# Optimization experiments

Measured on AMD Instinct MI355X. Metric: run time of the kernel, lower is better.

Reference implementation:

```python
import jax, jax.numpy as jnp
import numpy as np

D_MODEL = 1024
D_STATE = 128
SEQ_LEN = 4096
BATCH = 4
N_FFT = 2 ** int(np.ceil(np.log2(2 * SEQ_LEN - 1)))  # 8192
LN_EPS = 1e-3  # keras LayerNormalization default epsilon


def setup_inputs() -> dict:
    key = jax.random.key(0)
    ks = jax.random.split(key, 12)
    def dense_w(k, fan_in, fan_out):
        lim = np.sqrt(6.0 / (fan_in + fan_out)).astype(np.float32)  # glorot uniform
        return jax.random.uniform(k, (fan_in, fan_out), jnp.float32, -lim, lim)
    return {
        "x": jax.random.normal(ks[0], (BATCH, SEQ_LEN, D_MODEL), jnp.float32),
        "ln_gamma": jnp.ones((D_MODEL,), jnp.float32),
        "ln_beta": jnp.zeros((D_MODEL,), jnp.float32),
        "W_in": dense_w(ks[1], D_MODEL, D_MODEL),
        "b_in": jnp.zeros((D_MODEL,), jnp.float32),
        "W_xs": dense_w(ks[2], D_MODEL, D_STATE),
        "W_B": dense_w(ks[3], D_MODEL, D_STATE),
        "b_B": jnp.zeros((D_STATE,), jnp.float32),
        "W_C": dense_w(ks[4], D_MODEL, D_STATE),
        "b_C": jnp.zeros((D_STATE,), jnp.float32),
        "A_log": jax.random.uniform(ks[5], (D_STATE,), jnp.float32, -4.0, -1.0),
        "D": jnp.ones((D_MODEL,), jnp.float32),
        "W_so": dense_w(ks[6], D_STATE, D_MODEL),
        "W_out": dense_w(ks[7], D_MODEL, D_MODEL),
        "b_out": jnp.zeros((D_MODEL,), jnp.float32),
    }


def reference(x, ln_gamma, ln_beta, W_in, b_in, W_xs, W_B, b_B, W_C, b_C,
              A_log, D, W_so, W_out, b_out):
    residual = x
    # LayerNorm over last dim
    mu = jnp.mean(x, axis=-1, keepdims=True)
    var = jnp.mean(jnp.square(x - mu), axis=-1, keepdims=True)
    xn = (x - mu) * jax.lax.rsqrt(var + LN_EPS) * ln_gamma + ln_beta
    # projections
    z = xn @ W_in + b_in                      # [B, L, d_model]
    x_state = z @ W_xs                        # [B, L, d_state]
    B_sel = z @ W_B + b_B                     # [B, L, d_state]
    C_sel = z @ W_C + b_C                     # [B, L, d_state]
    # stable A-parameterization -> kernel K[t, s] = exp(A_s * t)
    A = -jnp.exp(A_log)                       # [d_state]
    t = jnp.arange(SEQ_LEN, dtype=jnp.float32)
    K = jnp.exp(t[:, None] * A[None, :])      # [L, d_state]
    # FFT convolution along time axis (zero-padded to N_FFT, causal slice)
    u = x_state * B_sel                       # [B, L, d_state]
    u_f = jnp.fft.rfft(u, n=N_FFT, axis=1)    # [B, N_FFT//2+1, d_state]
    k_f = jnp.fft.rfft(K, n=N_FFT, axis=0)    # [N_FFT//2+1, d_state]
    y_state = jnp.fft.irfft(u_f * k_f[None], n=N_FFT, axis=1)[:, :SEQ_LEN]
    y_state = y_state * C_sel
    # output path with skip connection through D
    y = y_state @ W_so + D * z                # [B, L, d_model]
    y = y @ W_out + b_out
    return y + residual
```

## Files before the change

### kernel.cpp

```cpp
#include <hip/hip_runtime.h>
#include <math.h>

#define D_MODEL 1024
#define D_STATE 128
#define SEQ_LEN 4096
#define BATCH 4
#define NTOK (BATCH * SEQ_LEN)
#define LN_EPS 1e-3f
#define NCHUNK 128
#define LCHUNK (SEQ_LEN / NCHUNK)

typedef __attribute__((ext_vector_type(8))) short bf16x8;
typedef __attribute__((ext_vector_type(4))) float f32x4;

__device__ __forceinline__ short f2bf(float f) {
    union { float f; unsigned u; } v; v.f = f;
    unsigned r = v.u + 0x7FFFu + ((v.u >> 16) & 1u);
    return (short)(r >> 16);
}
__device__ __forceinline__ float bf2f(short s) {
    union { unsigned u; float f; } v; v.u = ((unsigned)(unsigned short)s) << 16;
    return v.f;
}

__global__ __launch_bounds__(256) void ln_kernel(const float* __restrict__ x,
                                                 const float* __restrict__ gamma,
                                                 const float* __restrict__ beta,
                                                 short* __restrict__ xn_bf) {
    int row = blockIdx.x;
    const float4* xr = (const float4*)(x + (size_t)row * D_MODEL);
    float4 v = xr[threadIdx.x];
    float s1 = v.x + v.y + v.z + v.w;
    float s2 = v.x * v.x + v.y * v.y + v.z * v.z + v.w * v.w;
    for (int off = 32; off; off >>= 1) {
        s1 += __shfl_down(s1, off);
        s2 += __shfl_down(s2, off);
    }
    __shared__ float ls1[4], ls2[4];
    int wid = threadIdx.x >> 6, lane = threadIdx.x & 63;
    if (lane == 0) { ls1[wid] = s1; ls2[wid] = s2; }
    __syncthreads();
    s1 = ls1[0] + ls1[1] + ls1[2] + ls1[3];
    s2 = ls2[0] + ls2[1] + ls2[2] + ls2[3];
    float mu = s1 * (1.0f / D_MODEL);
    float var = s2 * (1.0f / D_MODEL) - mu * mu;
    float r = rsqrtf(var + LN_EPS);
    float4 g = ((const float4*)gamma)[threadIdx.x];
    float4 b = ((const float4*)beta)[threadIdx.x];
    short4 o;
    o.x = f2bf((v.x - mu) * r * g.x + b.x);
    o.y = f2bf((v.y - mu) * r * g.y + b.y);
    o.z = f2bf((v.z - mu) * r * g.z + b.z);
    o.w = f2bf((v.w - mu) * r * g.w + b.w);
    ((short4*)(xn_bf + (size_t)row * D_MODEL))[threadIdx.x] = o;
}

__global__ __launch_bounds__(256) void prep_kernel(
    const float* __restrict__ W_in, const float* __restrict__ W_xs,
    const float* __restrict__ W_B, const float* __restrict__ W_C,
    const float* __restrict__ W_so, const float* __restrict__ W_out,
    const float* __restrict__ bB, const float* __restrict__ bC,
    short* __restrict__ W_inT, short* __restrict__ W3T,
    short* __restrict__ W_soT, short* __restrict__ W_outT,
    float* __restrict__ bias3) {
    int blk = blockIdx.x;
    const float* in; short* out; int K, N, tile;
    if (blk < 1024)      { in = W_in;  out = W_inT;           K = 1024; N = 1024; tile = blk; }
    else if (blk < 1152) { in = W_xs;  out = W3T;             K = 1024; N = 128;  tile = blk - 1024; }
    else if (blk < 1280) { in = W_B;   out = W3T + 128*1024;  K = 1024; N = 128;  tile = blk - 1152; }
    else if (blk < 1408) { in = W_C;   out = W3T + 256*1024;  K = 1024; N = 128;  tile = blk - 1280; }
    else if (blk < 1536) { in = W_so;  out = W_soT;           K = 128;  N = 1024; tile = blk - 1408; }
    else if (blk < 2560) { in = W_out; out = W_outT;          K = 1024; N = 1024; tile = blk - 1536; }
    else {
        int t = threadIdx.y * 32 + threadIdx.x;
        for (int n = t; n < 384; n += 256)
            bias3[n] = (n < 128) ? 0.f : ((n < 256) ? bB[n - 128] : bC[n - 256]);
        return;
    }
    __shared__ float t32[32][33];
    int ntiles = N / 32;
    int nb = (tile % ntiles) * 32, kb = (tile / ntiles) * 32;
    int tx = threadIdx.x, ty = threadIdx.y;
#pragma unroll
    for (int i = 0; i < 4; ++i)
        t32[ty + 8 * i][tx] = in[(size_t)(kb + ty + 8 * i) * N + nb + tx];
    __syncthreads();
#pragma unroll
    for (int i = 0; i < 4; ++i)
        out[(size_t)(nb + ty + 8 * i) * K + kb + tx] = f2bf(t32[tx][ty + 8 * i]);
}

template<int HAS_BIAS, int HAS_ADD, int ADD_BF, int HAS_SCALE, int OUT_F32, int OUT_BF, int SWZ>
__global__ __launch_bounds__(256, 4) void gemm_bf16(
    const short* __restrict__ A, const short* __restrict__ BT,
    const float* __restrict__ bias,
    const float* __restrict__ addf, const short* __restrict__ addb,
    const float* __restrict__ addscale,
    float* __restrict__ Cf, short* __restrict__ Cbf,
    int Mt, int Nt, int K) {
    __shared__ short As[128 * 64];
    __shared__ short Bs[128 * 64];
    int p = blockIdx.x;
    int mtile, ntile;
    if (SWZ) {
        int k = p & 7, q = p >> 3;
        ntile = q & 7;
        mtile = k + 8 * (q >> 3);
    } else {
        mtile = p % Mt;
        ntile = p / Mt;
    }
    int m0 = mtile * 128, n0 = ntile * 128;
    int N = Nt * 128;
    int tid = threadIdx.x;
    int lane = tid & 63;
    int w = tid >> 6;
    int quad = lane >> 4, r16 = lane & 15;
    int wm = (w & 1) * 64, wn = (w >> 1) * 64;

    f32x4 acc[4][4] = {};

    for (int k0 = 0; k0 < K; k0 += 64) {
#pragma unroll
        for (int it = 0; it < 4; ++it) {
            int seg = it * 256 + tid;
            int row = seg >> 3, slot = seg & 7;
            int kc8 = slot ^ (row & 7);
            const short* gp = A + (size_t)(m0 + row) * K + k0 + kc8 * 8;
            __builtin_amdgcn_global_load_lds(
                (const __attribute__((address_space(1))) unsigned*)gp,
                (__attribute__((address_space(3))) unsigned*)(As + seg * 8), 16, 0, 0);
        }
#pragma unroll
        for (int it = 0; it < 4; ++it) {
            int seg = it * 256 + tid;
            int row = seg >> 3, slot = seg & 7;
            int kc8 = slot ^ (row & 7);
            const short* gp = BT + (size_t)(n0 + row) * K + k0 + kc8 * 8;
            __builtin_amdgcn_global_load_lds(
                (const __attribute__((address_space(1))) unsigned*)gp,
                (__attribute__((address_space(3))) unsigned*)(Bs + seg * 8), 16, 0, 0);
        }
        __syncthreads();

        const short* abase = As + (wm + r16) * 64;
        const short* bbase = Bs + (wn + r16) * 64;
        int sw = r16 & 7;
#pragma unroll
        for (int kk = 0; kk < 2; ++kk) {
            int phys = ((quad + 4 * kk) ^ sw) * 8;
            bf16x8 af[4], bfr[4];
#pragma unroll
            for (int i = 0; i < 4; ++i) af[i] = *(const bf16x8*)(abase + i * 16 * 64 + phys);
#pragma unroll
            for (int j = 0; j < 4; ++j) bfr[j] = *(const bf16x8*)(bbase + j * 16 * 64 + phys);
#pragma unroll
            for (int i = 0; i < 4; ++i)
#pragma unroll
                for (int j = 0; j < 4; ++j)
                    acc[i][j] = __builtin_amdgcn_mfma_f32_16x16x32_bf16(af[i], bfr[j], acc[i][j], 0, 0, 0);
        }
        __syncthreads();
    }

#pragma unroll
    for (int i = 0; i < 4; ++i) {
#pragma unroll
        for (int j = 0; j < 4; ++j) {
            int col = n0 + wn + j * 16 + r16;
            float bv = HAS_BIAS ? bias[col] : 0.f;
            float sc = HAS_SCALE ? addscale[col] : 1.f;
#pragma unroll
            for (int pr = 0; pr < 4; ++pr) {
                int row = m0 + wm + i * 16 + quad * 4 + pr;
                float v = acc[i][j][pr] + bv;
                if (HAS_ADD) {
                    float av = ADD_BF ? bf2f(addb[(size_t)row * N + col])
                                      : addf[(size_t)row * N + col];
                    v += sc * av;
                }
                if (OUT_F32) Cf[(size_t)row * N + col] = v;
                if (OUT_BF) Cbf[(size_t)row * N + col] = f2bf(v);
            }
        }
    }
}

__global__ __launch_bounds__(128) void scan_p1(const float* __restrict__ s3,
                                               const float* __restrict__ A_log,
                                               float* __restrict__ hbuf,
                                               float* __restrict__ Ebuf) {
    int s = threadIdx.x;
    int c = blockIdx.x, b = blockIdx.y;
    float a = expf(-expf(A_log[s]));
    float h = 0.f;
    size_t base = (size_t)b * SEQ_LEN + (size_t)c * LCHUNK;
#pragma unroll 8
    for (int i = 0; i < LCHUNK; ++i) {
        size_t r = base + i;
        float u = s3[r * 384 + s] * s3[r * 384 + 128 + s];
        h = a * h + u;
        hbuf[r * 128 + s] = h;
    }
    Ebuf[((size_t)b * NCHUNK + c) * 128 + s] = h;
}

__global__ __launch_bounds__(512) void scan_p2(const float* __restrict__ A_log,
                                               const float* __restrict__ Ebuf,
                                               float* __restrict__ Gbuf) {
    int tid = threadIdx.x;
    int b = tid >> 7, s = tid & 127;
    float pw = expf(-expf(A_log[s]) * (float)LCHUNK);
    float G = 0.f;
    for (int c0 = 0; c0 < NCHUNK; c0 += 16) {
        float e[16];
#pragma unroll
        for (int t = 0; t < 16; ++t)
            e[t] = Ebuf[((size_t)b * NCHUNK + c0 + t) * 128 + s];
#pragma unroll
        for (int t = 0; t < 16; ++t) {
            G = pw * G + e[t];
            Gbuf[((size_t)b * NCHUNK + c0 + t) * 128 + s] = G;
        }
    }
}

__global__ __launch_bounds__(128) void scan_p3(const float* __restrict__ s3,
                                               const float* __restrict__ A_log,
                                               const float* __restrict__ hbuf,
                                               const float* __restrict__ Gbuf,
                                               short* __restrict__ ys_bf) {
    int s = threadIdx.x;
    int c = blockIdx.x, b = blockIdx.y;
    float a = expf(-expf(A_log[s]));
    float carry = (c == 0) ? 0.f : Gbuf[((size_t)b * NCHUNK + c - 1) * 128 + s];
    float p = a;
    size_t base = (size_t)b * SEQ_LEN + (size_t)c * LCHUNK;
#pragma unroll 8
    for (int i = 0; i < LCHUNK; ++i) {
        size_t r = base + i;
        float h = hbuf[r * 128 + s] + p * carry;
        p *= a;
        ys_bf[r * 128 + s] = f2bf(h * s3[r * 384 + 256 + s]);
    }
}

extern "C" void kernel_launch(void* const* d_in, const int* in_sizes, int n_in,
                              void* d_out, int out_size, void* d_ws, size_t ws_size,
                              hipStream_t stream) {
    const float* x     = (const float*)d_in[0];
    const float* ln_g  = (const float*)d_in[1];
    const float* ln_b  = (const float*)d_in[2];
    const float* W_in  = (const float*)d_in[3];
    const float* b_in  = (const float*)d_in[4];
    const float* W_xs  = (const float*)d_in[5];
    const float* W_B   = (const float*)d_in[6];
    const float* b_B   = (const float*)d_in[7];
    const float* W_C   = (const float*)d_in[8];
    const float* b_C   = (const float*)d_in[9];
    const float* A_log = (const float*)d_in[10];
    const float* Dvec  = (const float*)d_in[11];
    const float* W_so  = (const float*)d_in[12];
    const float* W_out = (const float*)d_in[13];
    const float* b_out = (const float*)d_in[14];
    float* out = (float*)d_out;

    char* w = (char*)d_ws;
    size_t off = 0;
    short* xn_bf = (short*)(w + off);
    float* hbuf  = (float*)(w + off);
    short* ys_bf = (short*)(w + off + 8388608);
    off += (size_t)NTOK * D_MODEL * 2;
    short* z_bf  = (short*)(w + off);
    off += (size_t)NTOK * D_MODEL * 2;
    short* y1_bf = (short*)(w + off);
    off += (size_t)NTOK * D_MODEL * 2;
    float* s3    = (float*)(w + off); off += (size_t)NTOK * 384 * 4;
    float* Ebuf  = (float*)(w + off); off += (size_t)BATCH * NCHUNK * 128 * 4;
    float* Gbuf  = (float*)(w + off); off += (size_t)BATCH * NCHUNK * 128 * 4;
    short* W_inT  = (short*)(w + off); off += (size_t)D_MODEL * D_MODEL * 2;
    short* W3T    = (short*)(w + off); off += (size_t)384 * D_MODEL * 2;
    short* W_soT  = (short*)(w + off); off += (size_t)D_MODEL * D_STATE * 2;
    short* W_outT = (short*)(w + off); off += (size_t)D_MODEL * D_MODEL * 2;
    float* bias3  = (float*)(w + off); off += 2048;

    prep_kernel<<<2561, dim3(32, 8), 0, stream>>>(W_in, W_xs, W_B, W_C, W_so, W_out,
                                                  b_B, b_C, W_inT, W3T, W_soT, W_outT, bias3);

    ln_kernel<<<NTOK, 256, 0, stream>>>(x, ln_g, ln_b, xn_bf);

    const int Mt = NTOK / 128;
    gemm_bf16<1, 0, 0, 0, 0, 1, 1><<<Mt * 8, 256, 0, stream>>>(
        xn_bf, W_inT, b_in, nullptr, nullptr, nullptr,
        nullptr, z_bf, Mt, 8, D_MODEL);

    gemm_bf16<1, 0, 0, 0, 1, 0, 0><<<Mt * 3, 256, 0, stream>>>(
        z_bf, W3T, bias3, nullptr, nullptr, nullptr,
        s3, nullptr, Mt, 3, D_MODEL);

    scan_p1<<<dim3(NCHUNK, BATCH), 128, 0, stream>>>(s3, A_log, hbuf, Ebuf);
    scan_p2<<<1, 512, 0, stream>>>(A_log, Ebuf, Gbuf);
    scan_p3<<<dim3(NCHUNK, BATCH), 128, 0, stream>>>(s3, A_log, hbuf, Gbuf, ys_bf);

    gemm_bf16<0, 1, 1, 1, 0, 1, 1><<<Mt * 8, 256, 0, stream>>>(
        ys_bf, W_soT, nullptr, nullptr, z_bf, Dvec,
        nullptr, y1_bf, Mt, 8, D_STATE);

    gemm_bf16<1, 1, 0, 0, 1, 0, 1><<<Mt * 8, 256, 0, stream>>>(
        y1_bf, W_outT, b_out, x, nullptr, nullptr,
        out, nullptr, Mt, 8, D_MODEL);
}
```

Baseline: 282.3 us.

## Add pipelined 256x256 tile GEMM with direct global-to-LDS loads for large projections

Adds a new bf16 MFMA GEMM kernel that uses 256x256 output tiles with 512 threads. It stages operands through double-buffered LDS via global_load_lds, using a swizzled layout and explicit vmcnt waits so loads for the next K-slice overlap the MFMAs on the current one. It also uses an XCD-aware tile mapping. Both 1024x1024 projections (W_in and W_out) switch to this kernel to get more data reuse per tile and hide more memory latency. The cost is higher register and LDS pressure (128 KB of LDS per block at 2 blocks per CU) and fragile hand-tuned wait counts.

```diff
diff --git a/kernel.cpp b/kernel.cpp
--- a/kernel.cpp
+++ b/kernel.cpp
@@ -186,6 +186,128 @@
     }
 }
 
+#define WAITV8 asm volatile("s_waitcnt vmcnt(8)" ::: "memory")
+#define WAITV4 asm volatile("s_waitcnt vmcnt(4)" ::: "memory")
+#define WAITV0 asm volatile("s_waitcnt vmcnt(0)" ::: "memory")
+#define SBARF  do { __builtin_amdgcn_s_barrier(); asm volatile("" ::: "memory"); } while (0)
+
+template<int HAS_BIAS, int HAS_ADD, int OUT_F32, int OUT_BF, int SWZ>
+__global__ __launch_bounds__(512, 2) void gemm256(
+    const short* __restrict__ A, const short* __restrict__ BT,
+    const float* __restrict__ bias, const float* __restrict__ addf,
+    float* __restrict__ Cf, short* __restrict__ Cbf,
+    int Mt, int Nt, int K) {
+    __shared__ short LA[2][2][8192];
+    __shared__ short LB[2][2][8192];
+    int p = blockIdx.x;
+    int mtile, ntile;
+    if (SWZ) {
+        int xcd = p & 7, q = p >> 3;
+        ntile = q % Nt;
+        mtile = xcd + 8 * (q / Nt);
+    } else {
+        mtile = p % Mt;
+        ntile = p / Mt;
+    }
+    int m0 = mtile * 256, n0 = ntile * 256;
+    int N = Nt * 256;
+    int tid = threadIdx.x;
+    int lane = tid & 63, w = tid >> 6;
+    int quad = lane >> 4, r16 = lane & 15;
+    int wm = w & 1, wn = w >> 1;
+    int nt = K >> 6;
+
+    f32x4 acc[8][4] = {};
+
+#define STG(TU, KK, ISB) do { \
+        const short* g_ = (ISB) ? BT : A; \
+        int rb_ = (ISB) ? n0 : m0; \
+        short* l_ = (ISB) ? &LB[(TU) & 1][KK][0] : &LA[(TU) & 1][KK][0]; \
+        _Pragma("unroll") \
+        for (int r_ = 0; r_ < 2; ++r_) { \
+            int seg_ = r_ * 512 + tid; \
+            int row_ = seg_ >> 2, sl_ = seg_ & 3; \
+            int kc_ = sl_ ^ ((row_ >> 1) & 3); \
+            const short* gp_ = g_ + (size_t)(rb_ + row_) * K + (TU) * 64 + (KK) * 32 + kc_ * 8; \
+            __builtin_amdgcn_global_load_lds( \
+                (const __attribute__((address_space(1))) unsigned*)gp_, \
+                (__attribute__((address_space(3))) unsigned*)(&l_[seg_ * 8]), 16, 0, 0); \
+        } \
+    } while (0)
+
+#define PH_LOADB(Bb) { _Pragma("unroll") for (int j_ = 0; j_ < 4; ++j_) \
+        bf[j_] = *(const bf16x8*)((Bb) + j_ * 512 + ph4); }
+#define PH_LOADA(Ab, IH) { _Pragma("unroll") for (int i_ = 0; i_ < 4; ++i_) \
+        af[i_] = *(const bf16x8*)((Ab) + (i_ + 4 * (IH)) * 512 + ph4); }
+#define PH_MFMA(IH) { __builtin_amdgcn_s_setprio(1); \
+        _Pragma("unroll") for (int i_ = 0; i_ < 4; ++i_) \
+        _Pragma("unroll") for (int j_ = 0; j_ < 4; ++j_) \
+            acc[i_ + 4 * (IH)][j_] = __builtin_amdgcn_mfma_f32_16x16x32_bf16( \
+                af[i_], bf[j_], acc[i_ + 4 * (IH)][j_], 0, 0, 0); \
+        __builtin_amdgcn_s_setprio(0); }
+
+    STG(0, 0, 0); STG(0, 0, 1); STG(0, 1, 0); STG(0, 1, 1); STG(1, 0, 0);
+
+    int ph4 = (quad ^ ((r16 >> 1) & 3)) * 8;
+    int arow = (wm << 7) + r16;
+    int brow = (wn << 6) + r16;
+    bf16x8 af[4], bf[4];
+
+    for (int t = 0; t + 1 < nt; ++t) {
+        int c = t & 1;
+        const short* Ab0 = &LA[c][0][arow * 32];
+        const short* Bb0 = &LB[c][0][brow * 32];
+        const short* Ab1 = &LA[c][1][arow * 32];
+        const short* Bb1 = &LB[c][1][brow * 32];
+        STG(t + 1, 0, 1);
+        WAITV8; SBARF;
+        PH_LOADB(Bb0); PH_LOADA(Ab0, 0); PH_MFMA(0);
+        STG(t + 1, 1, 0);
+        WAITV8; SBARF;
+        PH_LOADA(Ab0, 1); PH_MFMA(1);
+        STG(t + 1, 1, 1);
+        WAITV8; SBARF;
+        PH_LOADB(Bb1); PH_LOADA(Ab1, 0); PH_MFMA(0);
+        if (t + 2 < nt) STG(t + 2, 0, 0);
+        WAITV8; SBARF;
+        PH_LOADA(Ab1, 1); PH_MFMA(1);
+    }
+    {
+        int c = (nt - 1) & 1;
+        const short* Ab0 = &LA[c][0][arow * 32];
+        const short* Bb0 = &LB[c][0][brow * 32];
+        const short* Ab1 = &LA[c][1][arow * 32];
+        const short* Bb1 = &LB[c][1][brow * 32];
+        WAITV4; SBARF;
+        PH_LOADB(Bb0); PH_LOADA(Ab0, 0); PH_MFMA(0);
+        PH_LOADA(Ab0, 1); PH_MFMA(1);
+        WAITV0; SBARF;
+        PH_LOADB(Bb1); PH_LOADA(Ab1, 0); PH_MFMA(0);
+        PH_LOADA(Ab1, 1); PH_MFMA(1);
+    }
+#undef STG
+#undef PH_LOADB
+#undef PH_LOADA
+#undef PH_MFMA
+
+#pragma unroll
+    for (int i = 0; i < 8; ++i) {
+#pragma unroll
+        for (int j = 0; j < 4; ++j) {
+            int col = n0 + wn * 64 + j * 16 + r16;
+            float bv = HAS_BIAS ? bias[col] : 0.f;
+#pragma unroll
+            for (int pr = 0; pr < 4; ++pr) {
+                int row = m0 + wm * 128 + i * 16 + quad * 4 + pr;
+                float v = acc[i][j][pr] + bv;
+                if (HAS_ADD) v += addf[(size_t)row * N + col];
+                if (OUT_F32) Cf[(size_t)row * N + col] = v;
+                if (OUT_BF) Cbf[(size_t)row * N + col] = f2bf(v);
+            }
+        }
+    }
+}
+
 __global__ __launch_bounds__(128) void scan_p1(const float* __restrict__ s3,
                                                const float* __restrict__ A_log,
                                                float* __restrict__ hbuf,
@@ -290,9 +412,10 @@
     ln_kernel<<<NTOK, 256, 0, stream>>>(x, ln_g, ln_b, xn_bf);
 
     const int Mt = NTOK / 128;
-    gemm_bf16<1, 0, 0, 0, 0, 1, 1><<<Mt * 8, 256, 0, stream>>>(
-        xn_bf, W_inT, b_in, nullptr, nullptr, nullptr,
-        nullptr, z_bf, Mt, 8, D_MODEL);
+    const int Mt2 = NTOK / 256;
+
+    gemm256<1, 0, 0, 1, 1><<<Mt2 * 4, 512, 0, stream>>>(
+        xn_bf, W_inT, b_in, nullptr, nullptr, z_bf, Mt2, 4, D_MODEL);
 
     gemm_bf16<1, 0, 0, 0, 1, 0, 0><<<Mt * 3, 256, 0, stream>>>(
         z_bf, W3T, bias3, nullptr, nullptr, nullptr,
@@ -306,7 +429,6 @@
         ys_bf, W_soT, nullptr, nullptr, z_bf, Dvec,
         nullptr, y1_bf, Mt, 8, D_STATE);
 
-    gemm_bf16<1, 1, 0, 0, 1, 0, 1><<<Mt * 8, 256, 0, stream>>>(
-        y1_bf, W_outT, b_out, x, nullptr, nullptr,
-        out, nullptr, Mt, 8, D_MODEL);
-}
+    gemm256<1, 1, 1, 0, 1><<<Mt2 * 4, 512, 0, stream>>>(
+        y1_bf, W_outT, b_out, x, out, nullptr, Mt2, 4, D_MODEL);
+}
```

Measured after the change: 297.4 us. +5.3%, slower.

## Pre-pack weights into MFMA fragment order and load B directly from global

Applied to the files above, without the earlier changes.

The weight transpose kernel now writes the bf16 weights in a blocked layout that matches the MFMA B-fragment order per 128x64 tile. The GEMM then drops the B shared-memory tile and reads B fragments straight from global memory (L2/L1) as 16-byte contiguous loads per lane. This halves LDS traffic and LDS footprint, which could raise occupancy. In exchange, B loads are now synchronous global reads inside the MFMA loop, so latency is exposed and shared B tiles are re-read by each wave from cache.

```diff
diff --git a/kernel.cpp b/kernel.cpp
--- a/kernel.cpp
+++ b/kernel.cpp
@@ -21,6 +21,11 @@
 __device__ __forceinline__ float bf2f(short s) {
     union { unsigned u; float f; } v; v.u = ((unsigned)(unsigned short)s) << 16;
     return v.f;
+}
+
+__device__ __forceinline__ size_t bpack_off(int n, int k, int K) {
+    return ((((size_t)(n >> 7) * (K >> 6) + (k >> 6)) * 2 + ((k >> 5) & 1)) * 8
+            + ((n & 127) >> 4)) * 512 + (size_t)(((k >> 3) & 3) * 128 + (n & 15) * 8 + (k & 7));
 }
 
 __global__ __launch_bounds__(256) void ln_kernel(const float* __restrict__ x,
@@ -86,8 +91,11 @@
         t32[ty + 8 * i][tx] = in[(size_t)(kb + ty + 8 * i) * N + nb + tx];
     __syncthreads();
 #pragma unroll
-    for (int i = 0; i < 4; ++i)
-        out[(size_t)(nb + ty + 8 * i) * K + kb + tx] = f2bf(t32[tx][ty + 8 * i]);
+    for (int i = 0; i < 4; ++i) {
+        int n = nb + ty + 8 * i;
+        int k = kb + tx;
+        out[bpack_off(n, k, K)] = f2bf(t32[tx][ty + 8 * i]);
+    }
 }
 
 template<int HAS_BIAS, int HAS_ADD, int ADD_BF, int HAS_SCALE, int OUT_F32, int OUT_BF, int SWZ>
@@ -99,7 +107,6 @@
     float* __restrict__ Cf, short* __restrict__ Cbf,
     int Mt, int Nt, int K) {
     __shared__ short As[128 * 64];
-    __shared__ short Bs[128 * 64];
     int p = blockIdx.x;
     int mtile, ntile;
     if (SWZ) {
@@ -117,10 +124,13 @@
     int w = tid >> 6;
     int quad = lane >> 4, r16 = lane & 15;
     int wm = (w & 1) * 64, wn = (w >> 1) * 64;
+    int wn4 = (w >> 1) * 4;
 
     f32x4 acc[4][4] = {};
 
-    for (int k0 = 0; k0 < K; k0 += 64) {
+    int kt = K >> 6;
+    for (int t = 0; t < kt; ++t) {
+        int k0 = t << 6;
 #pragma unroll
         for (int it = 0; it < 4; ++it) {
             int seg = it * 256 + tid;
@@ -131,29 +141,21 @@
                 (const __attribute__((address_space(1))) unsigned*)gp,
                 (__attribute__((address_space(3))) unsigned*)(As + seg * 8), 16, 0, 0);
         }
-#pragma unroll
-        for (int it = 0; it < 4; ++it) {
-            int seg = it * 256 + tid;
-            int row = seg >> 3, slot = seg & 7;
-            int kc8 = slot ^ (row & 7);
-            const short* gp = BT + (size_t)(n0 + row) * K + k0 + kc8 * 8;
-            __builtin_amdgcn_global_load_lds(
-                (const __attribute__((address_space(1))) unsigned*)gp,
-                (__attribute__((address_space(3))) unsigned*)(Bs + seg * 8), 16, 0, 0);
-        }
         __syncthreads();
 
+        int bbase = (((ntile * kt + t) * 2) * 8 + wn4) * 512 + lane * 8;
         const short* abase = As + (wm + r16) * 64;
-        const short* bbase = Bs + (wn + r16) * 64;
         int sw = r16 & 7;
 #pragma unroll
         for (int kk = 0; kk < 2; ++kk) {
+            bf16x8 bfr[4];
+#pragma unroll
+            for (int j = 0; j < 4; ++j)
+                bfr[j] = *(const bf16x8*)(BT + bbase + kk * 4096 + j * 512);
             int phys = ((quad + 4 * kk) ^ sw) * 8;
-            bf16x8 af[4], bfr[4];
+            bf16x8 af[4];
 #pragma unroll
             for (int i = 0; i < 4; ++i) af[i] = *(const bf16x8*)(abase + i * 16 * 64 + phys);
-#pragma unroll
-            for (int j = 0; j < 4; ++j) bfr[j] = *(const bf16x8*)(bbase + j * 16 * 64 + phys);
 #pragma unroll
             for (int i = 0; i < 4; ++i)
 #pragma unroll
```

Result: slower. 292.4 us (+3.6%).

## Merge LN into prep kernel and restructure chunked scan to drop hbuf and p2

Applied to the files above, without the earlier changes.

Folds the LayerNorm launch into the weight-prep kernel as extra blocks, removing one launch. The chunked scan no longer stores per-step partial states (hbuf) or runs the single-block carry pass. Instead, scan_p3 recomputes the local recurrence from s3 and derives each chunk's carry by scanning the preceding chunk totals itself. This removes the hbuf write and read traffic (about 8 MB each way) and a serial single-block kernel, at the cost of re-reading s3 and redundant carry prefix work, up to 127 steps per block.

```diff
diff --git a/kernel.cpp b/kernel.cpp
--- a/kernel.cpp
+++ b/kernel.cpp
@@ -23,47 +23,47 @@
     return v.f;
 }
 
-__global__ __launch_bounds__(256) void ln_kernel(const float* __restrict__ x,
-                                                 const float* __restrict__ gamma,
-                                                 const float* __restrict__ beta,
-                                                 short* __restrict__ xn_bf) {
-    int row = blockIdx.x;
-    const float4* xr = (const float4*)(x + (size_t)row * D_MODEL);
-    float4 v = xr[threadIdx.x];
-    float s1 = v.x + v.y + v.z + v.w;
-    float s2 = v.x * v.x + v.y * v.y + v.z * v.z + v.w * v.w;
-    for (int off = 32; off; off >>= 1) {
-        s1 += __shfl_down(s1, off);
-        s2 += __shfl_down(s2, off);
-    }
-    __shared__ float ls1[4], ls2[4];
-    int wid = threadIdx.x >> 6, lane = threadIdx.x & 63;
-    if (lane == 0) { ls1[wid] = s1; ls2[wid] = s2; }
-    __syncthreads();
-    s1 = ls1[0] + ls1[1] + ls1[2] + ls1[3];
-    s2 = ls2[0] + ls2[1] + ls2[2] + ls2[3];
-    float mu = s1 * (1.0f / D_MODEL);
-    float var = s2 * (1.0f / D_MODEL) - mu * mu;
-    float r = rsqrtf(var + LN_EPS);
-    float4 g = ((const float4*)gamma)[threadIdx.x];
-    float4 b = ((const float4*)beta)[threadIdx.x];
-    short4 o;
-    o.x = f2bf((v.x - mu) * r * g.x + b.x);
-    o.y = f2bf((v.y - mu) * r * g.y + b.y);
-    o.z = f2bf((v.z - mu) * r * g.z + b.z);
-    o.w = f2bf((v.w - mu) * r * g.w + b.w);
-    ((short4*)(xn_bf + (size_t)row * D_MODEL))[threadIdx.x] = o;
-}
-
-__global__ __launch_bounds__(256) void prep_kernel(
+__global__ __launch_bounds__(256) void prep_ln_kernel(
     const float* __restrict__ W_in, const float* __restrict__ W_xs,
     const float* __restrict__ W_B, const float* __restrict__ W_C,
     const float* __restrict__ W_so, const float* __restrict__ W_out,
     const float* __restrict__ bB, const float* __restrict__ bC,
     short* __restrict__ W_inT, short* __restrict__ W3T,
     short* __restrict__ W_soT, short* __restrict__ W_outT,
-    float* __restrict__ bias3) {
+    float* __restrict__ bias3,
+    const float* __restrict__ x, const float* __restrict__ gamma,
+    const float* __restrict__ beta, short* __restrict__ xn_bf) {
     int blk = blockIdx.x;
+    if (blk >= 2561) {
+        int row = blk - 2561;
+        int t = threadIdx.y * 32 + threadIdx.x;
+        const float4* xr = (const float4*)(x + (size_t)row * D_MODEL);
+        float4 v = xr[t];
+        float s1 = v.x + v.y + v.z + v.w;
+        float s2 = v.x * v.x + v.y * v.y + v.z * v.z + v.w * v.w;
+        for (int off = 32; off; off >>= 1) {
+            s1 += __shfl_down(s1, off);
+            s2 += __shfl_down(s2, off);
+        }
+        __shared__ float ls1[4], ls2[4];
+        int wid = t >> 6, lane = t & 63;
+        if (lane == 0) { ls1[wid] = s1; ls2[wid] = s2; }
+        __syncthreads();
+        s1 = ls1[0] + ls1[1] + ls1[2] + ls1[3];
+        s2 = ls2[0] + ls2[1] + ls2[2] + ls2[3];
+        float mu = s1 * (1.0f / D_MODEL);
+        float var = s2 * (1.0f / D_MODEL) - mu * mu;
+        float r = rsqrtf(var + LN_EPS);
+        float4 g = ((const float4*)gamma)[t];
+        float4 b = ((const float4*)beta)[t];
+        short4 o;
+        o.x = f2bf((v.x - mu) * r * g.x + b.x);
+        o.y = f2bf((v.y - mu) * r * g.y + b.y);
+        o.z = f2bf((v.z - mu) * r * g.z + b.z);
+        o.w = f2bf((v.w - mu) * r * g.w + b.w);
+        ((short4*)(xn_bf + (size_t)row * D_MODEL))[t] = o;
+        return;
+    }
     const float* in; short* out; int K, N, tile;
     if (blk < 1024)      { in = W_in;  out = W_inT;           K = 1024; N = 1024; tile = blk; }
     else if (blk < 1152) { in = W_xs;  out = W3T;             K = 1024; N = 128;  tile = blk - 1024; }
@@ -188,7 +188,6 @@
 
 __global__ __launch_bounds__(128) void scan_p1(const float* __restrict__ s3,
                                                const float* __restrict__ A_log,
-                                               float* __restrict__ hbuf,
                                                float* __restrict__ Ebuf) {
     int s = threadIdx.x;
     int c = blockIdx.x, b = blockIdx.y;
@@ -200,48 +199,42 @@
         size_t r = base + i;
         float u = s3[r * 384 + s] * s3[r * 384 + 128 + s];
         h = a * h + u;
-        hbuf[r * 128 + s] = h;
     }
     Ebuf[((size_t)b * NCHUNK + c) * 128 + s] = h;
-}
-
-__global__ __launch_bounds__(512) void scan_p2(const float* __restrict__ A_log,
-                                               const float* __restrict__ Ebuf,
-                                               float* __restrict__ Gbuf) {
-    int tid = threadIdx.x;
-    int b = tid >> 7, s = tid & 127;
-    float pw = expf(-expf(A_log[s]) * (float)LCHUNK);
-    float G = 0.f;
-    for (int c0 = 0; c0 < NCHUNK; c0 += 16) {
-        float e[16];
-#pragma unroll
-        for (int t = 0; t < 16; ++t)
-            e[t] = Ebuf[((size_t)b * NCHUNK + c0 + t) * 128 + s];
-#pragma unroll
-        for (int t = 0; t < 16; ++t) {
-            G = pw * G + e[t];
-            Gbuf[((size_t)b * NCHUNK + c0 + t) * 128 + s] = G;
-        }
-    }
 }
 
 __global__ __launch_bounds__(128) void scan_p3(const float* __restrict__ s3,
                                                const float* __restrict__ A_log,
-                                               const float* __restrict__ hbuf,
-                                               const float* __restrict__ Gbuf,
+                                               const float* __restrict__ Ebuf,
                                                short* __restrict__ ys_bf) {
     int s = threadIdx.x;
     int c = blockIdx.x, b = blockIdx.y;
-    float a = expf(-expf(A_log[s]));
-    float carry = (c == 0) ? 0.f : Gbuf[((size_t)b * NCHUNK + c - 1) * 128 + s];
-    float p = a;
+    float al = -expf(A_log[s]);
+    float a = expf(al);
+    float pw = expf(al * (float)LCHUNK);
+    float G = 0.f;
+    const float* Eb = Ebuf + (size_t)b * NCHUNK * 128 + s;
+    int c0 = 0;
+    for (; c0 + 16 <= c; c0 += 16) {
+        float e[16];
+#pragma unroll
+        for (int t = 0; t < 16; ++t) e[t] = Eb[(size_t)(c0 + t) * 128];
+#pragma unroll
+        for (int t = 0; t < 16; ++t) G = pw * G + e[t];
+    }
+    for (; c0 < c; ++c0) G = pw * G + Eb[(size_t)c0 * 128];
+    float carry = G;
+
+    float h = 0.f, p = a;
     size_t base = (size_t)b * SEQ_LEN + (size_t)c * LCHUNK;
 #pragma unroll 8
     for (int i = 0; i < LCHUNK; ++i) {
         size_t r = base + i;
-        float h = hbuf[r * 128 + s] + p * carry;
+        float u = s3[r * 384 + s] * s3[r * 384 + 128 + s];
+        h = a * h + u;
+        float hv = h + p * carry;
         p *= a;
-        ys_bf[r * 128 + s] = f2bf(h * s3[r * 384 + 256 + s]);
+        ys_bf[r * 128 + s] = f2bf(hv * s3[r * 384 + 256 + s]);
     }
 }
 
@@ -268,7 +261,6 @@
     char* w = (char*)d_ws;
     size_t off = 0;
     short* xn_bf = (short*)(w + off);
-    float* hbuf  = (float*)(w + off);
     short* ys_bf = (short*)(w + off + 8388608);
     off += (size_t)NTOK * D_MODEL * 2;
     short* z_bf  = (short*)(w + off);
@@ -277,17 +269,16 @@
     off += (size_t)NTOK * D_MODEL * 2;
     float* s3    = (float*)(w + off); off += (size_t)NTOK * 384 * 4;
     float* Ebuf  = (float*)(w + off); off += (size_t)BATCH * NCHUNK * 128 * 4;
-    float* Gbuf  = (float*)(w + off); off += (size_t)BATCH * NCHUNK * 128 * 4;
     short* W_inT  = (short*)(w + off); off += (size_t)D_MODEL * D_MODEL * 2;
     short* W3T    = (short*)(w + off); off += (size_t)384 * D_MODEL * 2;
     short* W_soT  = (short*)(w + off); off += (size_t)D_MODEL * D_STATE * 2;
     short* W_outT = (short*)(w + off); off += (size_t)D_MODEL * D_MODEL * 2;
     float* bias3  = (float*)(w + off); off += 2048;
 
-    prep_kernel<<<2561, dim3(32, 8), 0, stream>>>(W_in, W_xs, W_B, W_C, W_so, W_out,
-                                                  b_B, b_C, W_inT, W3T, W_soT, W_outT, bias3);
-
-    ln_kernel<<<NTOK, 256, 0, stream>>>(x, ln_g, ln_b, xn_bf);
+    prep_ln_kernel<<<2561 + NTOK, dim3(32, 8), 0, stream>>>(
+        W_in, W_xs, W_B, W_C, W_so, W_out, b_B, b_C,
+        W_inT, W3T, W_soT, W_outT, bias3,
+        x, ln_g, ln_b, xn_bf);
 
     const int Mt = NTOK / 128;
     gemm_bf16<1, 0, 0, 0, 0, 1, 1><<<Mt * 8, 256, 0, stream>>>(
@@ -298,9 +289,8 @@
         z_bf, W3T, bias3, nullptr, nullptr, nullptr,
         s3, nullptr, Mt, 3, D_MODEL);
 
-    scan_p1<<<dim3(NCHUNK, BATCH), 128, 0, stream>>>(s3, A_log, hbuf, Ebuf);
-    scan_p2<<<1, 512, 0, stream>>>(A_log, Ebuf, Gbuf);
-    scan_p3<<<dim3(NCHUNK, BATCH), 128, 0, stream>>>(s3, A_log, hbuf, Gbuf, ys_bf);
+    scan_p1<<<dim3(NCHUNK, BATCH), 128, 0, stream>>>(s3, A_log, Ebuf);
+    scan_p3<<<dim3(NCHUNK, BATCH), 128, 0, stream>>>(s3, A_log, Ebuf, ys_bf);
 
     gemm_bf16<0, 1, 1, 1, 0, 1, 1><<<Mt * 8, 256, 0, stream>>>(
         ys_bf, W_soT, nullptr, nullptr, z_bf, Dvec,
```

Result: no change. 285.0 us (+1.0%).
